# Optimization experiments

Measured on AMD Instinct MI355X. Metric: run time of the kernel, lower is better.

Reference implementation:

```python
import jax, jax.numpy as jnp
import numpy as np

NX, NU, NY, NW = 64, 32, 32, 64
B, T = 256, 2048


def setup_inputs() -> dict:
    key = jax.random.key(0)
    ks = jax.random.split(key, 11)

    def lin_w(k, out_f, in_f):
        # torch.nn.Linear default init scale ~ 1/sqrt(in_f)
        lim = 1.0 / np.sqrt(in_f)
        return jax.random.uniform(k, (out_f, in_f), jnp.float32, -lim, lim)

    return {
        "x_pred": jax.random.normal(ks[0], (B, T, NU), jnp.float32),
        # Y initialized as identity in the module; keep it well-conditioned
        "Y": jnp.eye(NX, dtype=jnp.float32) + 0.01 * jax.random.normal(ks[1], (NX, NX), jnp.float32),
        # lambdas initialized to ones; keep strictly positive
        "lambdas": 1.0 + 0.1 * jax.random.uniform(ks[2], (NW, 1), jnp.float32),
        "A": lin_w(ks[3], NX, NX),
        "B1": lin_w(ks[4], NX, NU),
        "B2": lin_w(ks[5], NX, NW),
        "C1": lin_w(ks[6], NY, NX),
        "D11": lin_w(ks[7], NY, NU),
        "D12": lin_w(ks[8], NY, NW),
        "C2": lin_w(ks[9], NW, NX),
        "D21": lin_w(ks[10], NW, NU),
    }


def reference(x_pred, Y, lambdas, A, B1, B2, C1, D11, D12, C2, D21):
    n_batch, n_sample, _ = x_pred.shape
    nx = A.shape[0]
    Y_inv = jnp.linalg.inv(Y)
    t_inv = 1.0 / jnp.squeeze(lambdas)  # diag of T_inv, [nw]

    x0 = jnp.zeros((n_batch, nx), x_pred.dtype)
    u_seq = jnp.swapaxes(x_pred, 0, 1)  # [T, B, nu]

    def step(x, u):
        # z = (C2_tilde x + D21_tilde u) @ T_inv ; T_inv diagonal -> column scale
        z = (x @ C2.T + u @ D21.T) * t_inv
        w = jnp.tanh(z)
        y_k = x @ C1.T + u @ D11.T + w @ D12.T
        x_next = (x @ A.T + u @ B1.T + w @ B2.T) @ Y_inv
        return x_next, y_k

    x_final, ys = jax.lax.scan(step, x0, u_seq)
    y = jnp.swapaxes(ys, 0, 1)  # [B, T, ny]
    return y, x_final
```

## Files before the change

### kernel.cpp

```cpp
#include <hip/hip_runtime.h>
#include <cstddef>

#define NXS 64
#define NUS 32
#define NYS 32
#define NWS 64
#define BBATCH 256
#define TT  2048

#define WS_WZT  0
#define WS_WXT  12288
#define WS_WYT  24576

typedef float v2f __attribute__((ext_vector_type(2)));

__device__ __forceinline__ float fast_tanh(float x) {
    float e = __expf(2.0f * x);
    return 1.0f - 2.0f * __builtin_amdgcn_rcpf(e + 1.0f);
}

template<int CTRL>
__device__ __forceinline__ float dpp_row_add(float v) {
    int t = __builtin_amdgcn_update_dpp(0, __float_as_int(v), CTRL, 0xF, 0xF, true);
    return v + __int_as_float(t);
}

__device__ __forceinline__ void step_barrier() {
    asm volatile("s_waitcnt lgkmcnt(0)\n\ts_barrier" ::: "memory");
}

__global__ __launch_bounds__(1024) void setup_kernel(const float* __restrict__ Y,
                                                     const float* __restrict__ lam,
                                                     const float* __restrict__ A,
                                                     const float* __restrict__ B1,
                                                     const float* __restrict__ B2,
                                                     const float* __restrict__ C1,
                                                     const float* __restrict__ D11,
                                                     const float* __restrict__ D12,
                                                     const float* __restrict__ C2,
                                                     const float* __restrict__ D21,
                                                     float* __restrict__ ws) {
    __shared__ float M[64 * 129];
    __shared__ float rowk[128];
    __shared__ float ck[64];
    __shared__ float WxL[96 * 64];
    __shared__ float WxwL[64 * 64];
    const int tid = threadIdx.x;

    for (int idx = tid; idx < 64 * 64; idx += 1024) {
        int r = idx >> 6, c = idx & 63;
        M[r * 129 + c]      = Y[idx];
        M[r * 129 + 64 + c] = (r == c) ? 1.0f : 0.0f;
    }
    __syncthreads();

    for (int k = 0; k < 64; ++k) {
        float dv = 1.0f / M[k * 129 + k];
        if (tid < 128) rowk[tid] = M[k * 129 + tid] * dv;
        if (tid >= 128 && tid < 192) ck[tid - 128] = M[(tid - 128) * 129 + k];
        __syncthreads();
        for (int idx = tid; idx < 64 * 128; idx += 1024) {
            int r = idx >> 7, c = idx & 127;
            float cur = M[r * 129 + c];
            M[r * 129 + c] = (r == k) ? rowk[c] : cur - ck[r] * rowk[c];
        }
        __syncthreads();
    }

    for (int idx = tid; idx < 6144; idx += 1024) {
        int k = idx >> 6, j = idx & 63;
        float s = 0.0f;
        if (k < 64) {
            #pragma unroll 8
            for (int m = 0; m < 64; ++m) s += A[m * 64 + k] * M[m * 129 + 64 + j];
        } else {
            int ku = k - 64;
            #pragma unroll 8
            for (int m = 0; m < 64; ++m) s += B1[m * 32 + ku] * M[m * 129 + 64 + j];
        }
        WxL[idx] = s;
        ws[WS_WXT + idx] = s;
    }
    for (int idx = tid; idx < 4096; idx += 1024) {
        int k = idx >> 6, j = idx & 63;
        float s = 0.0f;
        #pragma unroll 8
        for (int m = 0; m < 64; ++m) s += B2[m * 64 + k] * M[m * 129 + 64 + j];
        WxwL[idx] = s;
        ws[WS_WXT + 6144 + idx] = s;
    }
    for (int idx = tid; idx < 2048; idx += 1024)
        ws[WS_WXT + 10240 + idx] = 0.0f;
    for (int idx = tid; idx < 2048; idx += 1024) {
        int k = idx >> 6, j = idx & 63;
        ws[WS_WZT + 10240 + idx] = D21[j * 32 + k] / lam[j];
    }
    for (int idx = tid; idx < 5120; idx += 1024) {
        int k = idx >> 5, j = idx & 31;
        float v = (k < 64) ? C1[j * 64 + k]
                : (k < 96) ? D11[j * 32 + (k - 64)]
                           : D12[j * 64 + (k - 96)];
        ws[WS_WYT + idx] = v;
    }
    for (int idx = tid; idx < 1024; idx += 1024)
        ws[WS_WYT + 5120 + idx] = 0.0f;
    __syncthreads();

    for (int idx = tid; idx < 6144; idx += 1024) {
        int k = idx >> 6, j = idx & 63;
        float s = 0.0f;
        #pragma unroll 8
        for (int m = 0; m < 64; ++m) s += WxL[k * 64 + m] * C2[j * 64 + m];
        ws[WS_WZT + idx] = s / lam[j];
    }
    for (int idx = tid; idx < 4096; idx += 1024) {
        int k = idx >> 6, j = idx & 63;
        float s = 0.0f;
        #pragma unroll 8
        for (int m = 0; m < 64; ++m) s += WxwL[k * 64 + m] * C2[j * 64 + m];
        ws[WS_WZT + 6144 + idx] = s / lam[j];
    }
}

__global__ __launch_bounds__(512, 2) void rnn2_kernel(const float* __restrict__ xp,
                                                      const float* __restrict__ ws,
                                                      float* __restrict__ out) {
    const int b    = blockIdx.x;
    const int tid  = threadIdx.x;
    const int wv   = tid >> 6;
    const int lane = tid & 63;
    const int p    = lane & 15;
    const int o    = lane >> 4;
    const int sw   = (p >> 2) & 1;

    __shared__ __align__(16) float sbuf[2][128];
    __shared__ __align__(16) float sring[2][16][160];
    __shared__ __align__(16) float uR[32][32];

    const float* __restrict__ Wzt = ws + WS_WZT;
    const float* __restrict__ Wxt = ws + WS_WXT;
    const float* __restrict__ Wyt = ws + WS_WYT;

    const float4* __restrict__ xp4 = (const float4*)(xp + (size_t)b * (TT * NUS));
    const size_t yb   = (size_t)b * (TT * NYS);
    const size_t xoff = (size_t)BBATCH * TT * NYS;

    if (tid < 128) {
        int s = tid >> 3, q = tid & 7;
        *(float4*)&uR[s][q * 4] = xp4[s * 8 + q];
    } else if (tid < 136) {
        *(float4*)&uR[31][(tid - 128) * 4] = make_float4(0.f, 0.f, 0.f, 0.f);
    } else if (tid < 168) {
        ((float4*)&sbuf[1][0])[tid - 136] = make_float4(0.f, 0.f, 0.f, 0.f);
    }
    __syncthreads();

    const bool q1 = (p & 3) == 1, q2 = (p & 3) == 2, q3 = (p & 3) == 3;

    if (wv < 4) {
        const int g   = wv;
        const int rz  = 4 * g + o;
        const int jzb = 4 * rz;
        const int zo  = jzb + (p & 3);
        v2f wz2[4][4];
        #pragma unroll
        for (int k2 = 0; k2 < 4; ++k2) {
            int row = 8 * p + 2 * ((k2 + 2 * sw) & 3);
            int r0  = row + (row >= 64 ? 32 : 0);
            #pragma unroll
            for (int r = 0; r < 4; ++r)
                wz2[k2][r] = (v2f){ Wzt[r0 * 64 + jzb + r], Wzt[(r0 + 1) * 64 + jzb + r] };
        }
        v2f zu1[16], zu2[16];
        #pragma unroll
        for (int mm = 0; mm < 16; ++mm) {
            zu1[mm] = (v2f){ Wzt[(64  + 2 * mm) * 64 + lane], Wzt[(65  + 2 * mm) * 64 + lane] };
            zu2[mm] = (v2f){ Wzt[(160 + 2 * mm) * 64 + lane], Wzt[(161 + 2 * mm) * 64 + lane] };
        }

        float4 ucz[8];
        auto ringZ = [&](int e, bool usecache) {
            const float4* P = (const float4*)uR[(e - 1) & 31];
            const float4* C = (const float4*)uR[e & 31];
            v2f a = (v2f){0.f, 0.f};
            #pragma unroll
            for (int q = 0; q < 8; ++q) {
                float4 up = usecache ? ucz[q] : P[q];
                float4 uc = C[q];
                a += (v2f){up.x, up.y} * zu1[2 * q] + (v2f){up.z, up.w} * zu1[2 * q + 1];
                a += (v2f){uc.x, uc.y} * zu2[2 * q] + (v2f){uc.z, uc.w} * zu2[2 * q + 1];
                ucz[q] = uc;
            }
            sring[(e >> 4) & 1][e & 15][lane] = a.x + a.y;
        };

        #pragma unroll
        for (int j = 0; j < 4; ++j) ringZ(4 * g + j, false);
        __syncthreads();

        float4 ufetch;
        for (int c = 0; c < TT / 16; ++c) {
            #pragma unroll
            for (int off = 0; off < 16; ++off) {
                const int rp = (off + 1) & 1, wp = off & 1;
                if (off == 0 && tid < 128 && c + 1 < TT / 16) {
                    int s = 16 * (c + 1) + (tid >> 3);
                    ufetch = xp4[s * 8 + (tid & 7)];
                }
                if (off == 4 && tid < 128 && c + 1 < TT / 16) {
                    int s = 16 * (c + 1) + (tid >> 3);
                    *(float4*)&uR[s & 31][(tid & 7) * 4] = ufetch;
                }
                if (off == 5 || off == 8 || off == 11 || off == 14)
                    ringZ(16 * (c + 1) + 4 * g + (off - 5) / 3, off != 5);

                const float4* sb4 = (const float4*)&sbuf[rp][0];
                float4 Ra = sb4[2 * p + sw];
                float4 Rb = sb4[2 * p + 1 - sw];
                v2f av[4] = { {Ra.x, Ra.y}, {Ra.z, Ra.w}, {Rb.x, Rb.y}, {Rb.z, Rb.w} };
                v2f c0 = {0.f, 0.f}, c1 = c0, c2 = c0, c3 = c0;
                #pragma unroll
                for (int k2 = 0; k2 < 4; ++k2) {
                    c0 += av[k2] * wz2[k2][0]; c1 += av[k2] * wz2[k2][1];
                    c2 += av[k2] * wz2[k2][2]; c3 += av[k2] * wz2[k2][3];
                }
                float h0 = c0.x + c0.y, h1 = c1.x + c1.y, h2 = c2.x + c2.y, h3 = c3.x + c3.y;
                h0 = dpp_row_add<0xB1>(h0); h0 = dpp_row_add<0x4E>(h0);
                h1 = dpp_row_add<0xB1>(h1); h1 = dpp_row_add<0x4E>(h1);
                h2 = dpp_row_add<0xB1>(h2); h2 = dpp_row_add<0x4E>(h2);
                h3 = dpp_row_add<0xB1>(h3); h3 = dpp_row_add<0x4E>(h3);
                float dz = h0;
                dz = q1 ? h1 : dz; dz = q2 ? h2 : dz; dz = q3 ? h3 : dz;
                dz = dpp_row_add<0x124>(dz); dz = dpp_row_add<0x128>(dz);
                float gst = sring[c & 1][off][zo];
                float wvv = fast_tanh(dz + gst);
                if (p < 4) sbuf[wp][64 + zo] = wvv;
                step_barrier();
            }
        }
    } else {
        const int g    = wv - 4;
        const int rx   = 4 * g + o;
        const int jxb  = 4 * rx;
        const int jyb  = 2 * rx;
        const int xo   = (p < 4) ? (64 + jxb + (p & 3)) : (128 + jyb + (p & 1));
        const int ycol = jyb + (p & 1);
        const bool qy  = (p & 1) != 0;
        v2f wx2[4][4], wy2[4][2];
        #pragma unroll
        for (int k2 = 0; k2 < 4; ++k2) {
            int row = 8 * p + 2 * ((k2 + 2 * sw) & 3);
            int r0  = row + (row >= 64 ? 32 : 0);
            #pragma unroll
            for (int r = 0; r < 4; ++r)
                wx2[k2][r] = (v2f){ Wxt[r0 * 64 + jxb + r], Wxt[(r0 + 1) * 64 + jxb + r] };
            wy2[k2][0] = (v2f){ Wyt[r0 * 32 + jyb],     Wyt[(r0 + 1) * 32 + jyb] };
            wy2[k2][1] = (v2f){ Wyt[r0 * 32 + jyb + 1], Wyt[(r0 + 1) * 32 + jyb + 1] };
        }
        const int l31 = lane & 31;
        v2f xu[16], yu[16];
        #pragma unroll
        for (int mm = 0; mm < 16; ++mm) {
            xu[mm] = (v2f){ Wxt[(64 + 2 * mm) * 64 + lane], Wxt[(65 + 2 * mm) * 64 + lane] };
            yu[mm] = (v2f){ Wyt[(64 + 2 * mm) * 32 + l31],  Wyt[(65 + 2 * mm) * 32 + l31] };
        }

        auto ringX = [&](int e) {
            const float4* P = (const float4*)uR[(e - 1) & 31];
            v2f ax = (v2f){0.f, 0.f}, ay = ax;
            #pragma unroll
            for (int q = 0; q < 8; ++q) {
                float4 up = P[q];
                v2f u0 = {up.x, up.y}, u1 = {up.z, up.w};
                ax += u0 * xu[2 * q] + u1 * xu[2 * q + 1];
                ay += u0 * yu[2 * q] + u1 * yu[2 * q + 1];
            }
            const int nb = (e >> 4) & 1, sl = e & 15;
            sring[nb][sl][64 + lane] = ax.x + ax.y;
            if (lane < 32) sring[nb][sl][128 + lane] = ay.x + ay.y;
        };

        #pragma unroll
        for (int j = 0; j < 4; ++j) ringX(4 * g + j);
        __syncthreads();

        float ybat[16];

        auto computeX = [&](const float* Sb, float& dxo, float& dyo) {
            const float4* sb4 = (const float4*)Sb;
            float4 Ra = sb4[2 * p + sw];
            float4 Rb = sb4[2 * p + 1 - sw];
            v2f av[4] = { {Ra.x, Ra.y}, {Ra.z, Ra.w}, {Rb.x, Rb.y}, {Rb.z, Rb.w} };
            v2f c0 = {0.f, 0.f}, c1 = c0, c2 = c0, c3 = c0, d0 = c0, d1 = c0;
            #pragma unroll
            for (int k2 = 0; k2 < 4; ++k2) {
                c0 += av[k2] * wx2[k2][0]; c1 += av[k2] * wx2[k2][1];
                c2 += av[k2] * wx2[k2][2]; c3 += av[k2] * wx2[k2][3];
                d0 += av[k2] * wy2[k2][0]; d1 += av[k2] * wy2[k2][1];
            }
            float h0 = c0.x + c0.y, h1 = c1.x + c1.y, h2 = c2.x + c2.y, h3 = c3.x + c3.y;
            float e0 = d0.x + d0.y, e1 = d1.x + d1.y;
            h0 = dpp_row_add<0xB1>(h0); h0 = dpp_row_add<0x4E>(h0);
            h1 = dpp_row_add<0xB1>(h1); h1 = dpp_row_add<0x4E>(h1);
            h2 = dpp_row_add<0xB1>(h2); h2 = dpp_row_add<0x4E>(h2);
            h3 = dpp_row_add<0xB1>(h3); h3 = dpp_row_add<0x4E>(h3);
            e0 = dpp_row_add<0xB1>(e0); e0 = dpp_row_add<0x4E>(e0);
            e1 = dpp_row_add<0xB1>(e1); e1 = dpp_row_add<0x4E>(e1);
            float dx = h0;
            dx = q1 ? h1 : dx; dx = q2 ? h2 : dx; dx = q3 ? h3 : dx;
            dx = dpp_row_add<0x124>(dx); dx = dpp_row_add<0x128>(dx);
            float dy = qy ? e1 : e0;
            dy = dpp_row_add<0x124>(dy); dy = dpp_row_add<0x128>(dy);
            dxo = dx; dyo = dy;
        };

        for (int c = 0; c < TT / 16; ++c) {
            #pragma unroll
            for (int off = 0; off < 16; ++off) {
                const int rp = (off + 1) & 1, wp = off & 1;
                if (off == 6 || off == 9 || off == 12 || off == 15)
                    ringX(16 * (c + 1) + 4 * g + (off - 6) / 3);
                float gst = sring[c & 1][off][xo];
                float dx, dy;
                computeX(&sbuf[rp][0], dx, dy);
                if (p < 4) sbuf[wp][jxb + (p & 3)] = dx + gst;
                ybat[(off + 15) & 15] = dy + gst;
                if (off == 0 && c >= 1 && (p == 4 || p == 5)) {
                    size_t base = yb + (size_t)(16 * c - 16) * NYS + ycol;
                    #pragma unroll
                    for (int s = 0; s < 16; ++s) out[base + (size_t)s * NYS] = ybat[s];
                }
                step_barrier();
            }
        }

        {
            float gst = sring[0][0][xo];
            float dx, dy;
            computeX(&sbuf[1][0], dx, dy);
            if (p < 4) out[xoff + (size_t)b * 64 + jxb + (p & 3)] = dx + gst;
            ybat[15] = dy + gst;
            if (p == 4 || p == 5) {
                size_t base = yb + (size_t)(TT - 16) * NYS + ycol;
                #pragma unroll
                for (int s = 0; s < 16; ++s) out[base + (size_t)s * NYS] = ybat[s];
            }
        }
    }
}

extern "C" void kernel_launch(void* const* d_in, const int* in_sizes, int n_in,
                              void* d_out, int out_size, void* d_ws, size_t ws_size,
                              hipStream_t stream) {
    const float* xp  = (const float*)d_in[0];
    const float* Y   = (const float*)d_in[1];
    const float* lam = (const float*)d_in[2];
    const float* A   = (const float*)d_in[3];
    const float* B1  = (const float*)d_in[4];
    const float* B2  = (const float*)d_in[5];
    const float* C1  = (const float*)d_in[6];
    const float* D11 = (const float*)d_in[7];
    const float* D12 = (const float*)d_in[8];
    const float* C2  = (const float*)d_in[9];
    const float* D21 = (const float*)d_in[10];
    float* out = (float*)d_out;
    float* ws  = (float*)d_ws;

    hipLaunchKernelGGL(setup_kernel, dim3(1), dim3(1024), 0, stream,
                       Y, lam, A, B1, B2, C1, D11, D12, C2, D21, ws);
    hipLaunchKernelGGL(rnn2_kernel, dim3(BBATCH), dim3(512), 0, stream, xp, ws, out);
}
```

Measured before the change: 1.083 ms.

## Process two batch sequences per block to interleave independent recurrences

Each block now handles two batch elements, and every wave runs the recurrence step for both sequences between the same barriers. Shared buffers, input prefetch and ring precompute are duplicated per sequence, and the grid is halved. The aim is to hide the serial latency of each timestep (DPP reductions, tanh, barrier) behind the second independent sequence and to halve the number of barriers per batch element. In exchange each wave does twice the work per step, the ringZ cache of the previous input row is dropped, and the grid shrinks to 128 blocks on a 256-CU device, which lowers parallelism.

```diff
diff --git a/kernel.cpp b/kernel.cpp
--- a/kernel.cpp
+++ b/kernel.cpp
@@ -122,10 +122,10 @@
     }
 }
 
-__global__ __launch_bounds__(512, 2) void rnn2_kernel(const float* __restrict__ xp,
+__global__ __launch_bounds__(512, 2) void rnn3_kernel(const float* __restrict__ xp,
                                                       const float* __restrict__ ws,
                                                       float* __restrict__ out) {
-    const int b    = blockIdx.x;
+    const int b0   = blockIdx.x * 2;
     const int tid  = threadIdx.x;
     const int wv   = tid >> 6;
     const int lane = tid & 63;
@@ -133,25 +133,37 @@
     const int o    = lane >> 4;
     const int sw   = (p >> 2) & 1;
 
-    __shared__ __align__(16) float sbuf[2][128];
-    __shared__ __align__(16) float sring[2][16][160];
-    __shared__ __align__(16) float uR[32][32];
+    __shared__ __align__(16) float sbuf[2][2][128];
+    __shared__ __align__(16) float sring[2][2][16][160];
+    __shared__ __align__(16) float uR[2][32][32];
 
     const float* __restrict__ Wzt = ws + WS_WZT;
     const float* __restrict__ Wxt = ws + WS_WXT;
     const float* __restrict__ Wyt = ws + WS_WYT;
 
-    const float4* __restrict__ xp4 = (const float4*)(xp + (size_t)b * (TT * NUS));
-    const size_t yb   = (size_t)b * (TT * NYS);
+    const float4* __restrict__ xp4A = (const float4*)(xp + (size_t)b0 * (TT * NUS));
+    const float4* __restrict__ xp4B = (const float4*)(xp + (size_t)(b0 + 1) * (TT * NUS));
+    const size_t ybA  = (size_t)b0 * (TT * NYS);
+    const size_t ybB  = (size_t)(b0 + 1) * (TT * NYS);
     const size_t xoff = (size_t)BBATCH * TT * NYS;
 
-    if (tid < 128) {
-        int s = tid >> 3, q = tid & 7;
-        *(float4*)&uR[s][q * 4] = xp4[s * 8 + q];
-    } else if (tid < 136) {
-        *(float4*)&uR[31][(tid - 128) * 4] = make_float4(0.f, 0.f, 0.f, 0.f);
-    } else if (tid < 168) {
-        ((float4*)&sbuf[1][0])[tid - 136] = make_float4(0.f, 0.f, 0.f, 0.f);
+    {
+        const float4 z4 = make_float4(0.f, 0.f, 0.f, 0.f);
+        if (tid < 128) {
+            int s = tid >> 3, q = tid & 7;
+            *(float4*)&uR[0][s][q * 4] = xp4A[s * 8 + q];
+        } else if (tid < 256) {
+            int t = tid - 128, s = t >> 3, q = t & 7;
+            *(float4*)&uR[1][s][q * 4] = xp4B[s * 8 + q];
+        } else if (tid < 264) {
+            *(float4*)&uR[0][31][(tid - 256) * 4] = z4;
+        } else if (tid < 272) {
+            *(float4*)&uR[1][31][(tid - 264) * 4] = z4;
+        } else if (tid < 304) {
+            ((float4*)&sbuf[0][1][0])[tid - 272] = z4;
+        } else if (tid < 336) {
+            ((float4*)&sbuf[1][1][0])[tid - 304] = z4;
+        }
     }
     __syncthreads();
 
@@ -178,63 +190,73 @@
             zu2[mm] = (v2f){ Wzt[(160 + 2 * mm) * 64 + lane], Wzt[(161 + 2 * mm) * 64 + lane] };
         }
 
-        float4 ucz[8];
-        auto ringZ = [&](int e, bool usecache) {
-            const float4* P = (const float4*)uR[(e - 1) & 31];
-            const float4* C = (const float4*)uR[e & 31];
+        auto ringZ = [&](int ch, int e) {
+            const float4* P = (const float4*)uR[ch][(e - 1) & 31];
+            const float4* C = (const float4*)uR[ch][e & 31];
             v2f a = (v2f){0.f, 0.f};
             #pragma unroll
             for (int q = 0; q < 8; ++q) {
-                float4 up = usecache ? ucz[q] : P[q];
+                float4 up = P[q];
                 float4 uc = C[q];
                 a += (v2f){up.x, up.y} * zu1[2 * q] + (v2f){up.z, up.w} * zu1[2 * q + 1];
                 a += (v2f){uc.x, uc.y} * zu2[2 * q] + (v2f){uc.z, uc.w} * zu2[2 * q + 1];
-                ucz[q] = uc;
-            }
-            sring[(e >> 4) & 1][e & 15][lane] = a.x + a.y;
+            }
+            sring[ch][(e >> 4) & 1][e & 15][lane] = a.x + a.y;
         };
 
         #pragma unroll
-        for (int j = 0; j < 4; ++j) ringZ(4 * g + j, false);
+        for (int j = 0; j < 4; ++j) { ringZ(0, 4 * g + j); ringZ(1, 4 * g + j); }
         __syncthreads();
 
+        auto stepZ = [&](int ch, int rp, int wp, float gst) {
+            const float4* sb4 = (const float4*)&sbuf[ch][rp][0];
+            float4 Ra = sb4[2 * p + sw];
+            float4 Rb = sb4[2 * p + 1 - sw];
+            v2f av[4] = { {Ra.x, Ra.y}, {Ra.z, Ra.w}, {Rb.x, Rb.y}, {Rb.z, Rb.w} };
+            v2f c0 = {0.f, 0.f}, c1 = c0, c2 = c0, c3 = c0;
+            #pragma unroll
+            for (int k2 = 0; k2 < 4; ++k2) {
+                c0 += av[k2] * wz2[k2][0]; c1 += av[k2] * wz2[k2][1];
+                c2 += av[k2] * wz2[k2][2]; c3 += av[k2] * wz2[k2][3];
+            }
+            float h0 = c0.x + c0.y, h1 = c1.x + c1.y, h2 = c2.x + c2.y, h3 = c3.x + c3.y;
+            h0 = dpp_row_add<0xB1>(h0); h0 = dpp_row_add<0x4E>(h0);
+            h1 = dpp_row_add<0xB1>(h1); h1 = dpp_row_add<0x4E>(h1);
+            h2 = dpp_row_add<0xB1>(h2); h2 = dpp_row_add<0x4E>(h2);
+            h3 = dpp_row_add<0xB1>(h3); h3 = dpp_row_add<0x4E>(h3);
+            float dz = h0;
+            dz = q1 ? h1 : dz; dz = q2 ? h2 : dz; dz = q3 ? h3 : dz;
+            dz = dpp_row_add<0x124>(dz); dz = dpp_row_add<0x128>(dz);
+            float wvv = fast_tanh(dz + gst);
+            if (p < 4) sbuf[ch][wp][64 + zo] = wvv;
+        };
+
+        const int chf = g >> 1;
+        const float4* __restrict__ xpf = (chf == 0) ? xp4A : xp4B;
+        const int t7 = tid & 127;
         float4 ufetch;
+
         for (int c = 0; c < TT / 16; ++c) {
             #pragma unroll
             for (int off = 0; off < 16; ++off) {
                 const int rp = (off + 1) & 1, wp = off & 1;
-                if (off == 0 && tid < 128 && c + 1 < TT / 16) {
-                    int s = 16 * (c + 1) + (tid >> 3);
-                    ufetch = xp4[s * 8 + (tid & 7)];
+                if (off == 0 && c + 1 < TT / 16) {
+                    int s = 16 * (c + 1) + (t7 >> 3);
+                    ufetch = xpf[s * 8 + (t7 & 7)];
                 }
-                if (off == 4 && tid < 128 && c + 1 < TT / 16) {
-                    int s = 16 * (c + 1) + (tid >> 3);
-                    *(float4*)&uR[s & 31][(tid & 7) * 4] = ufetch;
+                if (off == 4 && c + 1 < TT / 16) {
+                    int s = 16 * (c + 1) + (t7 >> 3);
+                    *(float4*)&uR[chf][s & 31][(t7 & 7) * 4] = ufetch;
                 }
                 if (off == 5 || off == 8 || off == 11 || off == 14)
-                    ringZ(16 * (c + 1) + 4 * g + (off - 5) / 3, off != 5);
-
-                const float4* sb4 = (const float4*)&sbuf[rp][0];
-                float4 Ra = sb4[2 * p + sw];
-                float4 Rb = sb4[2 * p + 1 - sw];
-                v2f av[4] = { {Ra.x, Ra.y}, {Ra.z, Ra.w}, {Rb.x, Rb.y}, {Rb.z, Rb.w} };
-                v2f c0 = {0.f, 0.f}, c1 = c0, c2 = c0, c3 = c0;
-                #pragma unroll
-                for (int k2 = 0; k2 < 4; ++k2) {
-                    c0 += av[k2] * wz2[k2][0]; c1 += av[k2] * wz2[k2][1];
-                    c2 += av[k2] * wz2[k2][2]; c3 += av[k2] * wz2[k2][3];
-                }
-                float h0 = c0.x + c0.y, h1 = c1.x + c1.y, h2 = c2.x + c2.y, h3 = c3.x + c3.y;
-                h0 = dpp_row_add<0xB1>(h0); h0 = dpp_row_add<0x4E>(h0);
-                h1 = dpp_row_add<0xB1>(h1); h1 = dpp_row_add<0x4E>(h1);
-                h2 = dpp_row_add<0xB1>(h2); h2 = dpp_row_add<0x4E>(h2);
-                h3 = dpp_row_add<0xB1>(h3); h3 = dpp_row_add<0x4E>(h3);
-                float dz = h0;
-                dz = q1 ? h1 : dz; dz = q2 ? h2 : dz; dz = q3 ? h3 : dz;
-                dz = dpp_row_add<0x124>(dz); dz = dpp_row_add<0x128>(dz);
-                float gst = sring[c & 1][off][zo];
-                float wvv = fast_tanh(dz + gst);
-                if (p < 4) sbuf[wp][64 + zo] = wvv;
+                    ringZ(0, 16 * (c + 1) + 4 * g + (off - 5) / 3);
+                if (off == 6 || off == 9 || off == 12 || off == 15)
+                    ringZ(1, 16 * (c + 1) + 4 * g + (off - 6) / 3);
+
+                float gstA = sring[0][c & 1][off][zo];
+                float gstB = sring[1][c & 1][off][zo];
+                stepZ(0, rp, wp, gstA);
+                stepZ(1, rp, wp, gstB);
                 step_barrier();
             }
         }
@@ -265,8 +287,8 @@
             yu[mm] = (v2f){ Wyt[(64 + 2 * mm) * 32 + l31],  Wyt[(65 + 2 * mm) * 32 + l31] };
         }
 
-        auto ringX = [&](int e) {
-            const float4* P = (const float4*)uR[(e - 1) & 31];
+        auto ringX = [&](int ch, int e) {
+            const float4* P = (const float4*)uR[ch][(e - 1) & 31];
             v2f ax = (v2f){0.f, 0.f}, ay = ax;
             #pragma unroll
             for (int q = 0; q < 8; ++q) {
@@ -276,15 +298,15 @@
                 ay += u0 * yu[2 * q] + u1 * yu[2 * q + 1];
             }
             const int nb = (e >> 4) & 1, sl = e & 15;
-            sring[nb][sl][64 + lane] = ax.x + ax.y;
-            if (lane < 32) sring[nb][sl][128 + lane] = ay.x + ay.y;
+            sring[ch][nb][sl][64 + lane] = ax.x + ax.y;
+            if (lane < 32) sring[ch][nb][sl][128 + lane] = ay.x + ay.y;
         };
 
         #pragma unroll
-        for (int j = 0; j < 4; ++j) ringX(4 * g + j);
+        for (int j = 0; j < 4; ++j) { ringX(0, 4 * g + j); ringX(1, 4 * g + j); }
         __syncthreads();
 
-        float ybat[16];
+        float ybatA[16], ybatB[16];
 
         auto computeX = [&](const float* Sb, float& dxo, float& dyo) {
             const float4* sb4 = (const float4*)Sb;
@@ -318,32 +340,55 @@
             #pragma unroll
             for (int off = 0; off < 16; ++off) {
                 const int rp = (off + 1) & 1, wp = off & 1;
+                if (off == 5 || off == 8 || off == 11 || off == 14)
+                    ringX(0, 16 * (c + 1) + 4 * g + (off - 5) / 3);
                 if (off == 6 || off == 9 || off == 12 || off == 15)
-                    ringX(16 * (c + 1) + 4 * g + (off - 6) / 3);
-                float gst = sring[c & 1][off][xo];
-                float dx, dy;
-                computeX(&sbuf[rp][0], dx, dy);
-                if (p < 4) sbuf[wp][jxb + (p & 3)] = dx + gst;
-                ybat[(off + 15) & 15] = dy + gst;
+                    ringX(1, 16 * (c + 1) + 4 * g + (off - 6) / 3);
+
+                float gstA = sring[0][c & 1][off][xo];
+                float gstB = sring[1][c & 1][off][xo];
+                float dxA, dyA, dxB, dyB;
+                computeX(&sbuf[0][rp][0], dxA, dyA);
+                computeX(&sbuf[1][rp][0], dxB, dyB);
+                if (p < 4) {
+                    sbuf[0][wp][jxb + (p & 3)] = dxA + gstA;
+                    sbuf[1][wp][jxb + (p & 3)] = dxB + gstB;
+                }
+                ybatA[(off + 15) & 15] = dyA + gstA;
+                ybatB[(off + 15) & 15] = dyB + gstB;
                 if (off == 0 && c >= 1 && (p == 4 || p == 5)) {
-                    size_t base = yb + (size_t)(16 * c - 16) * NYS + ycol;
+                    size_t baseA = ybA + (size_t)(16 * c - 16) * NYS + ycol;
+                    size_t baseB = ybB + (size_t)(16 * c - 16) * NYS + ycol;
                     #pragma unroll
-                    for (int s = 0; s < 16; ++s) out[base + (size_t)s * NYS] = ybat[s];
+                    for (int s = 0; s < 16; ++s) {
+                        out[baseA + (size_t)s * NYS] = ybatA[s];
+                        out[baseB + (size_t)s * NYS] = ybatB[s];
+                    }
                 }
                 step_barrier();
             }
         }
 
         {
-            float gst = sring[0][0][xo];
-            float dx, dy;
-            computeX(&sbuf[1][0], dx, dy);
-            if (p < 4) out[xoff + (size_t)b * 64 + jxb + (p & 3)] = dx + gst;
-            ybat[15] = dy + gst;
+            float gstA = sring[0][0][0][xo];
+            float gstB = sring[1][0][0][xo];
+            float dxA, dyA, dxB, dyB;
+            computeX(&sbuf[0][1][0], dxA, dyA);
+            computeX(&sbuf[1][1][0], dxB, dyB);
+            if (p < 4) {
+                out[xoff + (size_t)b0 * 64 + jxb + (p & 3)]       = dxA + gstA;
+                out[xoff + (size_t)(b0 + 1) * 64 + jxb + (p & 3)] = dxB + gstB;
+            }
+            ybatA[15] = dyA + gstA;
+            ybatB[15] = dyB + gstB;
             if (p == 4 || p == 5) {
-                size_t base = yb + (size_t)(TT - 16) * NYS + ycol;
+                size_t baseA = ybA + (size_t)(TT - 16) * NYS + ycol;
+                size_t baseB = ybB + (size_t)(TT - 16) * NYS + ycol;
                 #pragma unroll
-                for (int s = 0; s < 16; ++s) out[base + (size_t)s * NYS] = ybat[s];
+                for (int s = 0; s < 16; ++s) {
+                    out[baseA + (size_t)s * NYS] = ybatA[s];
+                    out[baseB + (size_t)s * NYS] = ybatB[s];
+                }
             }
         }
     }
@@ -368,5 +413,5 @@
 
     hipLaunchKernelGGL(setup_kernel, dim3(1), dim3(1024), 0, stream,
                        Y, lam, A, B1, B2, C1, D11, D12, C2, D21, ws);
-    hipLaunchKernelGGL(rnn2_kernel, dim3(BBATCH), dim3(512), 0, stream, xp, ws, out);
-}
+    hipLaunchKernelGGL(rnn3_kernel, dim3(BBATCH / 2), dim3(512), 0, stream, xp, ws, out);
+}
```

Measured after the change: 1.544 ms. 1.43x slower.
